# Performance work log

Hardware: AMD Instinct MI355X
Metric: run time of the kernel (lower is better)

## Reference

```python
import jax, jax.numpy as jnp
import numpy as np

N = 30000      # num nodes
E = 600000     # num edges
D = 128        # feature dim (all layers)
R = 7          # num_relation
G = 16         # num graphs in batch
L = 3          # num layers (hidden_dims = [128,128,128])


def setup_inputs() -> dict:
    key = jax.random.key(0)
    ks = jax.random.split(key, 10)
    x = jax.random.normal(ks[0], (N, D), dtype=jnp.float32)
    node_in = jax.random.randint(ks[1], (E,), 0, N)
    node_out = jax.random.randint(ks[2], (E,), 0, N)
    relation = jax.random.randint(ks[3], (E,), 0, R)
    edge_weight = jax.random.uniform(ks[4], (E,), dtype=jnp.float32)
    node2graph = jnp.sort(jax.random.randint(ks[5], (N,), 0, G))
    # learned params: per-layer relational linear (R*D -> D) and self-loop linear (D -> D)
    Wr = jax.random.normal(ks[6], (L, R * D, D), dtype=jnp.float32) * 0.02
    br = jnp.zeros((L, D), dtype=jnp.float32)
    Wl = jax.random.normal(ks[7], (L, D, D), dtype=jnp.float32) * 0.02
    bl = jnp.zeros((L, D), dtype=jnp.float32)
    return dict(x=x, node_in=node_in, node_out=node_out, relation=relation,
                edge_weight=edge_weight, node2graph=node2graph,
                Wr=Wr, br=br, Wl=Wl, bl=bl)


def reference(x, node_in, node_out, relation, edge_weight, node2graph, Wr, br, Wl, bl):
    # relation-indexed destination segment: node_out * R + relation
    seg = node_out * R + relation            # (E,)
    ew = edge_weight[:, None]                # (E, 1)
    h = x
    for i in range(L):
        msg = h[node_in] * ew                                         # gather + weight, (E, D)
        upd = jax.ops.segment_sum(msg, seg, num_segments=N * R)       # scatter_add, (N*R, D)
        upd = upd.reshape(N, R * D)                                   # per-relation concat
        h = jax.nn.relu(upd @ Wr[i] + br[i] + h @ Wl[i] + bl[i])      # linear + self-loop + act
    node_feature = h                                                  # (N, D)
    graph_feature = jax.ops.segment_sum(node_feature, node2graph, num_segments=G)  # sum readout
    return graph_feature, node_feature
```

## Files before the change

### kernel.cpp

```cpp
#include <hip/hip_runtime.h>

#define NN 30000
#define NE 600000
#define DD 128
#define RR 7
#define GG 16
#define LL 3

typedef short bf16x8 __attribute__((ext_vector_type(8)));
typedef float f32x4  __attribute__((ext_vector_type(4)));

__device__ __forceinline__ unsigned short f2bf(float f) {
    unsigned u = __float_as_uint(f);
    unsigned r = (u + 0x7fffu + ((u >> 16) & 1u)) >> 16;
    return (unsigned short)r;
}
__device__ __forceinline__ float bf2f(unsigned short b) {
    return __uint_as_float(((unsigned)b) << 16);
}

__device__ __forceinline__ void gl_lds16(const void* g, void* l) {
    __builtin_amdgcn_global_load_lds(
        (const __attribute__((address_space(1))) void*)g,
        (__attribute__((address_space(3))) void*)l, 16, 0, 0);
}

__global__ __launch_bounds__(256) void pack_weights(
    const float* __restrict__ Wl,
    const float* __restrict__ Wr,
    unsigned short* __restrict__ Bw)
{
    int t = blockIdx.x * 256 + threadIdx.x;
    if (t >= LL * 1024 * DD) return;
    int l = t >> 17;
    int rem = t & 131071;
    int n = rem >> 7;
    int k = rem & 127;
    float v;
    if (n < DD) {
        v = Wl[(size_t)l * DD * DD + k * DD + n];
    } else {
        int q = n - DD;
        v = Wr[(size_t)l * RR * DD * DD + (size_t)((q >> 7) * DD + k) * DD + (q & 127)];
    }
    Bw[(size_t)l * 1024 * DD + n * DD + k] = f2bf(v);
}

__global__ __launch_bounds__(256) void convert_bf16(
    const float* __restrict__ in, unsigned short* __restrict__ out, int n4)
{
    int i = blockIdx.x * 256 + threadIdx.x;
    if (i >= n4) return;
    float4 v = ((const float4*)in)[i];
    ushort4 o;
    o.x = f2bf(v.x); o.y = f2bf(v.y); o.z = f2bf(v.z); o.w = f2bf(v.w);
    ((ushort4*)out)[i] = o;
}

#define ASTR 128
__global__ __launch_bounds__(256) void gemm_mfma(
    const unsigned short* __restrict__ hb,
    const unsigned short* __restrict__ Bw,
    const float* __restrict__ br,
    const float* __restrict__ bl,
    unsigned short* __restrict__ haccb,
    unsigned short* __restrict__ Zb,
    int N)
{
    __shared__ unsigned short As[64 * ASTR];
    __shared__ unsigned short Bs[128 * ASTR];

    const int tid  = threadIdx.x;
    const int wave = tid >> 6;
    const int lane = tid & 63;
    const int quad = lane >> 4;
    const int l16  = lane & 15;
    const int row0 = blockIdx.x * 64;
    const int col0 = blockIdx.y * 128;

#pragma unroll
    for (int i = 0; i < 4; ++i) {
        int g = i * 4 + wave;
        gl_lds16(hb + (size_t)(row0 + g * 4) * DD + lane * 8,
                 As + g * 512);
    }
#pragma unroll
    for (int i = 0; i < 8; ++i) {
        int g = i * 4 + wave;
        gl_lds16(Bw + (size_t)col0 * DD + (size_t)g * 512 + lane * 8,
                 Bs + g * 512);
    }
    __syncthreads();

    f32x4 acc[4][2];
#pragma unroll
    for (int mt = 0; mt < 4; ++mt)
#pragma unroll
        for (int nt = 0; nt < 2; ++nt)
            acc[mt][nt] = (f32x4){0.f, 0.f, 0.f, 0.f};

    const unsigned short* As_l = As + l16 * ASTR;
    const unsigned short* Bs_l = Bs + (wave * 32 + l16) * ASTR;

#pragma unroll
    for (int kc = 0; kc < 4; ++kc) {
        int ko = kc * 32 + quad * 8;
        bf16x8 a0 = *(const bf16x8*)(As_l + 0 * 16 * ASTR + ko);
        bf16x8 a1 = *(const bf16x8*)(As_l + 1 * 16 * ASTR + ko);
        bf16x8 a2 = *(const bf16x8*)(As_l + 2 * 16 * ASTR + ko);
        bf16x8 a3 = *(const bf16x8*)(As_l + 3 * 16 * ASTR + ko);
        bf16x8 b0 = *(const bf16x8*)(Bs_l + 0 * 16 * ASTR + ko);
        bf16x8 b1 = *(const bf16x8*)(Bs_l + 1 * 16 * ASTR + ko);
        acc[0][0] = __builtin_amdgcn_mfma_f32_16x16x32_bf16(a0, b0, acc[0][0], 0, 0, 0);
        acc[1][0] = __builtin_amdgcn_mfma_f32_16x16x32_bf16(a1, b0, acc[1][0], 0, 0, 0);
        acc[2][0] = __builtin_amdgcn_mfma_f32_16x16x32_bf16(a2, b0, acc[2][0], 0, 0, 0);
        acc[3][0] = __builtin_amdgcn_mfma_f32_16x16x32_bf16(a3, b0, acc[3][0], 0, 0, 0);
        acc[0][1] = __builtin_amdgcn_mfma_f32_16x16x32_bf16(a0, b1, acc[0][1], 0, 0, 0);
        acc[1][1] = __builtin_amdgcn_mfma_f32_16x16x32_bf16(a1, b1, acc[1][1], 0, 0, 0);
        acc[2][1] = __builtin_amdgcn_mfma_f32_16x16x32_bf16(a2, b1, acc[2][1], 0, 0, 0);
        acc[3][1] = __builtin_amdgcn_mfma_f32_16x16x32_bf16(a3, b1, acc[3][1], 0, 0, 0);
    }

    const int ncol = wave * 32 + l16;
    if (col0 == 0) {
        float bias0 = br[ncol] + bl[ncol];
        float bias1 = br[ncol + 16] + bl[ncol + 16];
#pragma unroll
        for (int mt = 0; mt < 4; ++mt) {
#pragma unroll
            for (int reg = 0; reg < 4; ++reg) {
                int row = row0 + mt * 16 + quad * 4 + reg;
                if (row < N) {
                    haccb[(size_t)row * DD + ncol]      = f2bf(acc[mt][0][reg] + bias0);
                    haccb[(size_t)row * DD + ncol + 16] = f2bf(acc[mt][1][reg] + bias1);
                }
            }
        }
    } else {
        const int zc = col0 - DD + ncol;
#pragma unroll
        for (int mt = 0; mt < 4; ++mt) {
#pragma unroll
            for (int reg = 0; reg < 4; ++reg) {
                int row = row0 + mt * 16 + quad * 4 + reg;
                if (row < N) {
                    Zb[(size_t)row * (RR * DD) + zc]      = f2bf(acc[mt][0][reg]);
                    Zb[(size_t)row * (RR * DD) + zc + 16] = f2bf(acc[mt][1][reg]);
                }
            }
        }
    }
}

__global__ __launch_bounds__(256) void edge_hist(
    const int* __restrict__ node_out, int* __restrict__ cnt, int E)
{
    int e = blockIdx.x * 256 + threadIdx.x;
    if (e < E) atomicAdd(&cnt[node_out[e]], 1);
}

__global__ __launch_bounds__(256) void scan_blk(
    const int* __restrict__ cnt, int* __restrict__ lscan,
    int* __restrict__ bsum, int N)
{
    __shared__ int s[256];
    int t = threadIdx.x;
    int i = blockIdx.x * 256 + t;
    int v = (i < N) ? cnt[i] : 0;
    s[t] = v;
    __syncthreads();
#pragma unroll
    for (int off = 1; off < 256; off <<= 1) {
        int u = (t >= off) ? s[t - off] : 0;
        __syncthreads();
        s[t] += u;
        __syncthreads();
    }
    if (i < N) lscan[i] = s[t] - v;
    if (t == 255) bsum[blockIdx.x] = s[255];
}

__global__ __launch_bounds__(128) void scan_bsum(
    int* __restrict__ bsum, int* __restrict__ boff, int nb)
{
    __shared__ int s[128];
    int t = threadIdx.x;
    int v = (t < nb) ? bsum[t] : 0;
    s[t] = v;
    __syncthreads();
#pragma unroll
    for (int off = 1; off < 128; off <<= 1) {
        int u = (t >= off) ? s[t - off] : 0;
        __syncthreads();
        s[t] += u;
        __syncthreads();
    }
    if (t < nb) boff[t] = s[t] - v;
}

__global__ __launch_bounds__(256) void scan_add(
    const int* __restrict__ lscan, const int* __restrict__ boff,
    int* __restrict__ start, int* __restrict__ cursor, int N)
{
    int i = blockIdx.x * 256 + threadIdx.x;
    if (i < N) {
        int v = lscan[i] + boff[i >> 8];
        start[i] = v;
        cursor[i] = v;
    }
    if (i == N) start[N] = NE;
}

__global__ __launch_bounds__(256) void edge_scatter_sort(
    const int* __restrict__ node_in,
    const int* __restrict__ node_out,
    const int* __restrict__ relation,
    const float* __restrict__ ew,
    int* __restrict__ cursor,
    int2* __restrict__ meta,
    int E)
{
    int e = blockIdx.x * 256 + threadIdx.x;
    if (e >= E) return;
    int no = node_out[e];
    int pos = atomicAdd(&cursor[no], 1);
    meta[pos] = make_int2(node_in[e] * (RR * DD) + relation[e] * DD,
                          __float_as_int(ew[e]));
}

__global__ __launch_bounds__(256) void aggregate(
    const unsigned short* __restrict__ Zb,
    const int* __restrict__ start,
    const int2* __restrict__ meta,
    const unsigned short* __restrict__ haccb,
    float* __restrict__ out_f32,
    unsigned short* __restrict__ out_bf16,
    int N)
{
    int wid = (blockIdx.x * 256 + threadIdx.x) >> 6;
    int lane = threadIdx.x & 63;
    if (wid >= N) return;

    int e0 = start[wid];
    int e1 = start[wid + 1];

    float accx = 0.f, accy = 0.f;
    int e = e0;
    for (; e + 8 <= e1; e += 8) {
        unsigned u[8]; float wt[8];
#pragma unroll
        for (int j = 0; j < 8; ++j) {
            int2 m = meta[e + j];
            u[j] = *(const unsigned*)(Zb + m.x + lane * 2);
            wt[j] = __int_as_float(m.y);
        }
#pragma unroll
        for (int j = 0; j < 8; ++j) {
            accx = fmaf(wt[j], __uint_as_float(u[j] << 16), accx);
            accy = fmaf(wt[j], __uint_as_float(u[j] & 0xffff0000u), accy);
        }
    }
    for (; e + 2 <= e1; e += 2) {
        int2 m0 = meta[e];
        int2 m1 = meta[e + 1];
        unsigned u0 = *(const unsigned*)(Zb + m0.x + lane * 2);
        unsigned u1 = *(const unsigned*)(Zb + m1.x + lane * 2);
        float w0 = __int_as_float(m0.y), w1 = __int_as_float(m1.y);
        accx = fmaf(w0, __uint_as_float(u0 << 16), accx);
        accy = fmaf(w0, __uint_as_float(u0 & 0xffff0000u), accy);
        accx = fmaf(w1, __uint_as_float(u1 << 16), accx);
        accy = fmaf(w1, __uint_as_float(u1 & 0xffff0000u), accy);
    }
    if (e < e1) {
        int2 m = meta[e];
        unsigned u = *(const unsigned*)(Zb + m.x + lane * 2);
        float wt = __int_as_float(m.y);
        accx = fmaf(wt, __uint_as_float(u << 16), accx);
        accy = fmaf(wt, __uint_as_float(u & 0xffff0000u), accy);
    }

    unsigned bu = *(const unsigned*)(haccb + (size_t)wid * DD + lane * 2);
    float ox = fmaxf(bf2f((unsigned short)(bu & 0xffffu)) + accx, 0.f);
    float oy = fmaxf(bf2f((unsigned short)(bu >> 16)) + accy, 0.f);
    if (out_f32) {
        *(float2*)(out_f32 + (size_t)wid * DD + lane * 2) = make_float2(ox, oy);
    }
    if (out_bf16) {
        ushort2 o; o.x = f2bf(ox); o.y = f2bf(oy);
        *(ushort2*)(out_bf16 + (size_t)wid * DD + lane * 2) = o;
    }
}

__global__ __launch_bounds__(256) void graph_sum(
    const float* __restrict__ nf,
    const int* __restrict__ n2g,
    float* __restrict__ gf,
    int N)
{
    int t = blockIdx.x * 256 + threadIdx.x;
    int chunk = t >> 5;
    int lane = t & 31;
    int n0 = chunk * 16;
    if (n0 >= N) return;
    int nend = n0 + 16; if (nend > N) nend = N;

    float4 acc = make_float4(0.f, 0.f, 0.f, 0.f);
    int curg = n2g[n0];
    for (int n = n0; n < nend; ++n) {
        int g = n2g[n];
        if (g != curg) {
            float* dst = gf + (size_t)curg * DD + lane * 4;
            atomicAdd(dst + 0, acc.x); atomicAdd(dst + 1, acc.y);
            atomicAdd(dst + 2, acc.z); atomicAdd(dst + 3, acc.w);
            acc = make_float4(0.f, 0.f, 0.f, 0.f);
            curg = g;
        }
        float4 v = *(const float4*)(nf + (size_t)n * DD + lane * 4);
        acc.x += v.x; acc.y += v.y; acc.z += v.z; acc.w += v.w;
    }
    float* dst = gf + (size_t)curg * DD + lane * 4;
    atomicAdd(dst + 0, acc.x); atomicAdd(dst + 1, acc.y);
    atomicAdd(dst + 2, acc.z); atomicAdd(dst + 3, acc.w);
}

extern "C" void kernel_launch(void* const* d_in, const int* in_sizes, int n_in,
                              void* d_out, int out_size, void* d_ws, size_t ws_size,
                              hipStream_t stream)
{
    const float* x        = (const float*)d_in[0];
    const int*   node_in  = (const int*)d_in[1];
    const int*   node_out = (const int*)d_in[2];
    const int*   relation = (const int*)d_in[3];
    const float* ew       = (const float*)d_in[4];
    const int*   n2g      = (const int*)d_in[5];
    const float* Wr       = (const float*)d_in[6];
    const float* br       = (const float*)d_in[7];
    const float* Wl       = (const float*)d_in[8];
    const float* bl       = (const float*)d_in[9];

    float* out = (float*)d_out;
    float* gf = out;
    float* nf = out + GG * DD;

    char* w = (char*)d_ws;
    unsigned short* Zb   = (unsigned short*)w; w += (size_t)NN * RR * DD * 2;
    unsigned short* haccb= (unsigned short*)w; w += (size_t)NN * DD * 2;
    unsigned short* hbA  = (unsigned short*)w; w += (size_t)NN * DD * 2;
    unsigned short* hbB  = (unsigned short*)w; w += (size_t)NN * DD * 2;
    unsigned short* Bw   = (unsigned short*)w; w += (size_t)LL * 1024 * DD * 2;
    int2*  meta   = (int2*)w;                  w += (size_t)NE * 8;
    int*   start  = (int*)w;                   w += (size_t)(NN + 1) * 4 + 60;
    int*   cursor = (int*)w;                   w += (size_t)NN * 4 + 64;
    int*   cnt    = (int*)w;                   w += (size_t)NN * 4 + 64;
    int*   lscan  = (int*)w;                   w += (size_t)NN * 4 + 64;
    int*   bsum   = (int*)w;                   w += 256 * 4;
    int*   boff   = (int*)w;                   w += 256 * 4;

    const int N = NN, E = NE;
    const int NB = (N + 255) / 256;

    pack_weights<<<(LL * 1024 * DD + 255) / 256, 256, 0, stream>>>(Wl, Wr, Bw);
    convert_bf16<<<(N * DD / 4 + 255) / 256, 256, 0, stream>>>(x, hbA, N * DD / 4);

    hipMemsetAsync(cnt, 0, (size_t)N * sizeof(int), stream);
    edge_hist<<<(E + 255) / 256, 256, 0, stream>>>(node_out, cnt, E);
    scan_blk<<<NB, 256, 0, stream>>>(cnt, lscan, bsum, N);
    scan_bsum<<<1, 128, 0, stream>>>(bsum, boff, NB);
    scan_add<<<(N + 256) / 256, 256, 0, stream>>>(lscan, boff, start, cursor, N);
    edge_scatter_sort<<<(E + 255) / 256, 256, 0, stream>>>(
        node_in, node_out, relation, ew, cursor, meta, E);

    dim3 ggrid((N + 63) / 64, 8);
    unsigned short* hin = hbA;
    unsigned short* hnext = hbB;
    for (int l = 0; l < LL; ++l) {
        const float* br_l = br + (size_t)l * DD;
        const float* bl_l = bl + (size_t)l * DD;
        const unsigned short* Bw_l = Bw + (size_t)l * 1024 * DD;

        gemm_mfma<<<ggrid, 256, 0, stream>>>(hin, Bw_l, br_l, bl_l, haccb, Zb, N);

        bool last = (l == LL - 1);
        aggregate<<<(N * 64 + 255) / 256, 256, 0, stream>>>(
            Zb, start, meta, haccb,
            last ? nf : (float*)nullptr,
            last ? (unsigned short*)nullptr : hnext, N);

        unsigned short* t = hin; hin = hnext; hnext = t;
    }

    hipMemsetAsync(gf, 0, (size_t)GG * DD * sizeof(float), stream);
    int chunks = (N + 15) / 16;
    graph_sum<<<(chunks * 32 + 255) / 256, 256, 0, stream>>>(nf, n2g, gf, N);
}
```

Before: 346.3 us.

## Replace per-node counting sort with two-level bucket sort of edges

Edge CSR construction is replaced: edges are first binned into 64-node buckets using padded global atomic counters, then a per-bucket block sorts them locally with LDS histogram and scan before writing meta and start offsets. This removes the three-kernel global scan and the heavily contended per-node atomics, at the cost of an extra temp buffer pass. BF16 conversions are also switched to the packed __float22bfloat162_rn intrinsic.

```diff
diff --git a/kernel.cpp b/kernel.cpp
--- a/kernel.cpp
+++ b/kernel.cpp
@@ -1,4 +1,5 @@
 #include <hip/hip_runtime.h>
+#include <hip/hip_bf16.h>
 
 #define NN 30000
 #define NE 600000
@@ -7,6 +8,8 @@
 #define GG 16
 #define LL 3
 
+#define NB64 ((NN + 63) / 64)
+
 typedef short bf16x8 __attribute__((ext_vector_type(8)));
 typedef float f32x4  __attribute__((ext_vector_type(4)));
 
@@ -17,6 +20,10 @@
 }
 __device__ __forceinline__ float bf2f(unsigned short b) {
     return __uint_as_float(((unsigned)b) << 16);
+}
+__device__ __forceinline__ ushort2 pk2bf(float a, float b) {
+    __hip_bfloat162 t = __float22bfloat162_rn(make_float2(a, b));
+    return *(ushort2*)&t;
 }
 
 __device__ __forceinline__ void gl_lds16(const void* g, void* l) {
@@ -52,9 +59,9 @@
     int i = blockIdx.x * 256 + threadIdx.x;
     if (i >= n4) return;
     float4 v = ((const float4*)in)[i];
-    ushort4 o;
-    o.x = f2bf(v.x); o.y = f2bf(v.y); o.z = f2bf(v.z); o.w = f2bf(v.w);
-    ((ushort4*)out)[i] = o;
+    ushort2 lo = pk2bf(v.x, v.y);
+    ushort2 hi = pk2bf(v.z, v.w);
+    ((ushort4*)out)[i] = make_ushort4(lo.x, lo.y, hi.x, hi.y);
 }
 
 #define ASTR 128
@@ -131,8 +138,10 @@
             for (int reg = 0; reg < 4; ++reg) {
                 int row = row0 + mt * 16 + quad * 4 + reg;
                 if (row < N) {
-                    haccb[(size_t)row * DD + ncol]      = f2bf(acc[mt][0][reg] + bias0);
-                    haccb[(size_t)row * DD + ncol + 16] = f2bf(acc[mt][1][reg] + bias1);
+                    ushort2 p = pk2bf(acc[mt][0][reg] + bias0,
+                                      acc[mt][1][reg] + bias1);
+                    haccb[(size_t)row * DD + ncol]      = p.x;
+                    haccb[(size_t)row * DD + ncol + 16] = p.y;
                 }
             }
         }
@@ -144,88 +153,109 @@
             for (int reg = 0; reg < 4; ++reg) {
                 int row = row0 + mt * 16 + quad * 4 + reg;
                 if (row < N) {
-                    Zb[(size_t)row * (RR * DD) + zc]      = f2bf(acc[mt][0][reg]);
-                    Zb[(size_t)row * (RR * DD) + zc + 16] = f2bf(acc[mt][1][reg]);
+                    ushort2 p = pk2bf(acc[mt][0][reg], acc[mt][1][reg]);
+                    Zb[(size_t)row * (RR * DD) + zc]      = p.x;
+                    Zb[(size_t)row * (RR * DD) + zc + 16] = p.y;
                 }
             }
         }
     }
 }
 
-__global__ __launch_bounds__(256) void edge_hist(
-    const int* __restrict__ node_out, int* __restrict__ cnt, int E)
+__global__ __launch_bounds__(256) void bucket_hist(
+    const int* __restrict__ node_out, int* __restrict__ bcnt, int E)
 {
     int e = blockIdx.x * 256 + threadIdx.x;
-    if (e < E) atomicAdd(&cnt[node_out[e]], 1);
-}
-
-__global__ __launch_bounds__(256) void scan_blk(
-    const int* __restrict__ cnt, int* __restrict__ lscan,
-    int* __restrict__ bsum, int N)
-{
-    __shared__ int s[256];
+    if (e < E) atomicAdd(&bcnt[(node_out[e] >> 6) * 16], 1);
+}
+
+__global__ __launch_bounds__(512) void bucket_scan(
+    const int* __restrict__ bcnt, int* __restrict__ bstart,
+    int* __restrict__ bcur, int nb)
+{
+    __shared__ int s[512];
     int t = threadIdx.x;
-    int i = blockIdx.x * 256 + t;
-    int v = (i < N) ? cnt[i] : 0;
+    int v = (t < nb) ? bcnt[t * 16] : 0;
     s[t] = v;
     __syncthreads();
 #pragma unroll
-    for (int off = 1; off < 256; off <<= 1) {
+    for (int off = 1; off < 512; off <<= 1) {
         int u = (t >= off) ? s[t - off] : 0;
         __syncthreads();
         s[t] += u;
         __syncthreads();
     }
-    if (i < N) lscan[i] = s[t] - v;
-    if (t == 255) bsum[blockIdx.x] = s[255];
-}
-
-__global__ __launch_bounds__(128) void scan_bsum(
-    int* __restrict__ bsum, int* __restrict__ boff, int nb)
-{
-    __shared__ int s[128];
-    int t = threadIdx.x;
-    int v = (t < nb) ? bsum[t] : 0;
-    s[t] = v;
-    __syncthreads();
-#pragma unroll
-    for (int off = 1; off < 128; off <<= 1) {
-        int u = (t >= off) ? s[t - off] : 0;
-        __syncthreads();
-        s[t] += u;
-        __syncthreads();
-    }
-    if (t < nb) boff[t] = s[t] - v;
-}
-
-__global__ __launch_bounds__(256) void scan_add(
-    const int* __restrict__ lscan, const int* __restrict__ boff,
-    int* __restrict__ start, int* __restrict__ cursor, int N)
-{
-    int i = blockIdx.x * 256 + threadIdx.x;
-    if (i < N) {
-        int v = lscan[i] + boff[i >> 8];
-        start[i] = v;
-        cursor[i] = v;
-    }
-    if (i == N) start[N] = NE;
-}
-
-__global__ __launch_bounds__(256) void edge_scatter_sort(
+    if (t <= nb) {
+        int excl = s[t] - v;
+        bstart[t] = excl;
+        if (t < nb) bcur[t * 16] = excl;
+    }
+}
+
+__global__ __launch_bounds__(256) void bucket_scatter(
     const int* __restrict__ node_in,
     const int* __restrict__ node_out,
     const int* __restrict__ relation,
     const float* __restrict__ ew,
-    int* __restrict__ cursor,
-    int2* __restrict__ meta,
+    int* __restrict__ bcur,
+    int2* __restrict__ tmp,
     int E)
 {
     int e = blockIdx.x * 256 + threadIdx.x;
     if (e >= E) return;
-    int no = node_out[e];
-    int pos = atomicAdd(&cursor[no], 1);
-    meta[pos] = make_int2(node_in[e] * (RR * DD) + relation[e] * DD,
-                          __float_as_int(ew[e]));
+    int o = node_out[e];
+    int pos = atomicAdd(&bcur[(o >> 6) * 16], 1);
+    tmp[pos] = make_int2(((o & 63) << 18) | (node_in[e] << 3) | relation[e],
+                         __float_as_int(ew[e]));
+}
+
+__global__ __launch_bounds__(256) void bucket_sort(
+    const int2* __restrict__ tmp,
+    const int* __restrict__ bstart,
+    int2* __restrict__ meta,
+    int* __restrict__ start,
+    int N)
+{
+    __shared__ int hist[64];
+    __shared__ int scan[64];
+    __shared__ int cur[64];
+    const int b = blockIdx.x;
+    const int t = threadIdx.x;
+    const int s0 = bstart[b];
+    const int s1 = bstart[b + 1];
+
+    if (t < 64) hist[t] = 0;
+    __syncthreads();
+    for (int i = s0 + t; i < s1; i += 256)
+        atomicAdd(&hist[((unsigned)tmp[i].x) >> 18], 1);
+    __syncthreads();
+
+    int v = (t < 64) ? hist[t] : 0;
+    if (t < 64) scan[t] = v;
+    __syncthreads();
+#pragma unroll
+    for (int off = 1; off < 64; off <<= 1) {
+        int u = (t < 64 && t >= off) ? scan[t - off] : 0;
+        __syncthreads();
+        if (t < 64) scan[t] += u;
+        __syncthreads();
+    }
+    if (t < 64) {
+        int excl = scan[t] - v;
+        cur[t] = s0 + excl;
+        int node = b * 64 + t;
+        if (node <= N) start[node] = s0 + excl;
+    }
+    __syncthreads();
+
+    for (int i = s0 + t; i < s1; i += 256) {
+        int2 m = tmp[i];
+        int j = ((unsigned)m.x) >> 18;
+        int pos = atomicAdd(&cur[j], 1);
+        int key = m.x & 0x3ffff;
+        int in = key >> 3, rel = key & 7;
+        meta[pos] = make_int2((in * RR + rel) << 7, m.y);
+    }
 }
 
 __global__ __launch_bounds__(256) void aggregate(
@@ -286,7 +316,7 @@
         *(float2*)(out_f32 + (size_t)wid * DD + lane * 2) = make_float2(ox, oy);
     }
     if (out_bf16) {
-        ushort2 o; o.x = f2bf(ox); o.y = f2bf(oy);
+        ushort2 o = pk2bf(ox, oy);
         *(ushort2*)(out_bf16 + (size_t)wid * DD + lane * 2) = o;
     }
 }
@@ -349,26 +379,23 @@
     unsigned short* hbB  = (unsigned short*)w; w += (size_t)NN * DD * 2;
     unsigned short* Bw   = (unsigned short*)w; w += (size_t)LL * 1024 * DD * 2;
     int2*  meta   = (int2*)w;                  w += (size_t)NE * 8;
+    int2*  tmp    = (int2*)w;                  w += (size_t)NE * 8;
     int*   start  = (int*)w;                   w += (size_t)(NN + 1) * 4 + 60;
-    int*   cursor = (int*)w;                   w += (size_t)NN * 4 + 64;
-    int*   cnt    = (int*)w;                   w += (size_t)NN * 4 + 64;
-    int*   lscan  = (int*)w;                   w += (size_t)NN * 4 + 64;
-    int*   bsum   = (int*)w;                   w += 256 * 4;
-    int*   boff   = (int*)w;                   w += 256 * 4;
+    int*   bcnt   = (int*)w;                   w += (size_t)NB64 * 16 * 4 + 64;
+    int*   bcur   = (int*)w;                   w += (size_t)NB64 * 16 * 4 + 64;
+    int*   bstart = (int*)w;                   w += (size_t)(NB64 + 1) * 4 + 60;
 
     const int N = NN, E = NE;
-    const int NB = (N + 255) / 256;
 
     pack_weights<<<(LL * 1024 * DD + 255) / 256, 256, 0, stream>>>(Wl, Wr, Bw);
     convert_bf16<<<(N * DD / 4 + 255) / 256, 256, 0, stream>>>(x, hbA, N * DD / 4);
 
-    hipMemsetAsync(cnt, 0, (size_t)N * sizeof(int), stream);
-    edge_hist<<<(E + 255) / 256, 256, 0, stream>>>(node_out, cnt, E);
-    scan_blk<<<NB, 256, 0, stream>>>(cnt, lscan, bsum, N);
-    scan_bsum<<<1, 128, 0, stream>>>(bsum, boff, NB);
-    scan_add<<<(N + 256) / 256, 256, 0, stream>>>(lscan, boff, start, cursor, N);
-    edge_scatter_sort<<<(E + 255) / 256, 256, 0, stream>>>(
-        node_in, node_out, relation, ew, cursor, meta, E);
+    hipMemsetAsync(bcnt, 0, (size_t)NB64 * 16 * sizeof(int), stream);
+    bucket_hist<<<(E + 255) / 256, 256, 0, stream>>>(node_out, bcnt, E);
+    bucket_scan<<<1, 512, 0, stream>>>(bcnt, bstart, bcur, NB64);
+    bucket_scatter<<<(E + 255) / 256, 256, 0, stream>>>(
+        node_in, node_out, relation, ew, bcur, tmp, E);
+    bucket_sort<<<NB64, 256, 0, stream>>>(tmp, bstart, meta, start, N);
 
     dim3 ggrid((N + 63) / 64, 8);
     unsigned short* hin = hbA;
```

After: 344.4 us. About the same (-0.5%).
